# Performance work log

Measured on AMD Instinct MI355X. Metric: run time of the kernel, lower is better.

## Reference

```python
import jax, jax.numpy as jnp
import numpy as np

D_MODEL = 1024
NUM_HEADS = 16
D_K = D_MODEL // NUM_HEADS
D_FF = 4096
EPS = 1e-5


def _layer_norm(x, g, b):
    mu = jnp.mean(x, axis=-1, keepdims=True)
    var = jnp.mean(jnp.square(x - mu), axis=-1, keepdims=True)
    return (x - mu) * jax.lax.rsqrt(var + EPS) * g + b


def setup_inputs() -> dict:
    key = jax.random.key(0)
    ks = jax.random.split(key, 16)
    s = 0.02
    inp = {
        "x": jax.random.normal(ks[0], (2, 2048, D_MODEL), dtype=jnp.float32),
        # attention projections, torch Linear convention: W [out, in]
        "wq": jax.random.normal(ks[1], (D_MODEL, D_MODEL), dtype=jnp.float32) * s,
        "bq": jnp.zeros((D_MODEL,), jnp.float32),
        "wk": jax.random.normal(ks[2], (D_MODEL, D_MODEL), dtype=jnp.float32) * s,
        "bk": jnp.zeros((D_MODEL,), jnp.float32),
        "wv": jax.random.normal(ks[3], (D_MODEL, D_MODEL), dtype=jnp.float32) * s,
        "bv": jnp.zeros((D_MODEL,), jnp.float32),
        "wo": jax.random.normal(ks[4], (D_MODEL, D_MODEL), dtype=jnp.float32) * s,
        "bo": jnp.zeros((D_MODEL,), jnp.float32),
        "ln1_g": jnp.ones((D_MODEL,), jnp.float32),
        "ln1_b": jnp.zeros((D_MODEL,), jnp.float32),
        "w1": jax.random.normal(ks[5], (D_FF, D_MODEL), dtype=jnp.float32) * s,
        "b1": jnp.zeros((D_FF,), jnp.float32),
        "w2": jax.random.normal(ks[6], (D_MODEL, D_FF), dtype=jnp.float32) * s,
        "b2": jnp.zeros((D_MODEL,), jnp.float32),
        "ln2_g": jnp.ones((D_MODEL,), jnp.float32),
        "ln2_b": jnp.zeros((D_MODEL,), jnp.float32),
    }
    return inp


def reference(x, wq, bq, wk, bk, wv, bv, wo, bo, ln1_g, ln1_b,
              w1, b1, w2, b2, ln2_g, ln2_b):
    B, S, D = x.shape
    H, Dk = NUM_HEADS, D_K
    # projections -> [B, H, S, Dk]
    q = (x @ wq.T + bq).reshape(B, S, H, Dk).transpose(0, 2, 1, 3)
    k = (x @ wk.T + bk).reshape(B, S, H, Dk).transpose(0, 2, 1, 3)
    v = (x @ wv.T + bv).reshape(B, S, H, Dk).transpose(0, 2, 1, 3)
    # explicit [B,H,S,S] scores (faithful to source, memory-bound)
    scores = jnp.einsum("bhqd,bhkd->bhqk", q, k) / jnp.sqrt(jnp.float32(Dk))
    attn = jax.nn.softmax(scores, axis=-1)
    ctx = jnp.einsum("bhqk,bhkd->bhqd", attn, v)
    ctx = ctx.transpose(0, 2, 1, 3).reshape(B, S, D)
    attn_out = _layer_norm(ctx @ wo.T + bo + x, ln1_g, ln1_b)
    # feed-forward (post-LN residual), GELU (erf, torch default)
    h = jax.nn.gelu(attn_out @ w1.T + b1, approximate=False)
    ff = h @ w2.T + b2
    return _layer_norm(ff + attn_out, ln2_g, ln2_b)
```

## Files before the change

### kernel.cpp

```cpp
#include <hip/hip_runtime.h>
#include <math.h>

#define DM   1024
#define SL   2048
#define NB   2
#define NH   16
#define DKH  64
#define DFF  4096
#define NTOK 4096

typedef unsigned short u16;
typedef unsigned int u32;
typedef __attribute__((ext_vector_type(8))) short bf16x8;
typedef __attribute__((ext_vector_type(4))) float f32x4;
typedef __attribute__((ext_vector_type(16))) float f32x16;

typedef __attribute__((address_space(1))) void gvoid;
typedef __attribute__((address_space(3))) void lvoid;

#define QSCALE 0.18033688011112042f

__device__ __forceinline__ u16 f2bf(float f) {
  union { float f; unsigned u; } v; v.f = f;
  unsigned r = (v.u + 0x7fffu + ((v.u >> 16) & 1u)) >> 16;
  return (u16)r;
}
__device__ __forceinline__ float bf2f(u16 h) {
  union { unsigned u; float f; } v; v.u = ((unsigned)h) << 16; return v.f;
}
__device__ __forceinline__ void gld16(const u16* g, u16* l) {
  __builtin_amdgcn_global_load_lds((gvoid*)g, (lvoid*)l, 16, 0, 0);
}

__global__ __launch_bounds__(256)
void cvt_all(const float* __restrict__ x,  const float* __restrict__ wq,
             const float* __restrict__ wk, const float* __restrict__ wv,
             const float* __restrict__ wo, const float* __restrict__ w1,
             const float* __restrict__ w2,
             u16* __restrict__ xb, u16* __restrict__ wqb, u16* __restrict__ wkb,
             u16* __restrict__ wvb, u16* __restrict__ wob, u16* __restrict__ w1b,
             u16* __restrict__ w2b) {
  const int total = 4194304;
  for (int i = blockIdx.x * blockDim.x + threadIdx.x; i < total;
       i += gridDim.x * blockDim.x) {
    const float* src; u16* dst; int off;
    if      (i < 1048576) { src = x;  dst = xb;  off = i; }
    else if (i < 1310720) { src = wq; dst = wqb; off = i - 1048576; }
    else if (i < 1572864) { src = wk; dst = wkb; off = i - 1310720; }
    else if (i < 1835008) { src = wv; dst = wvb; off = i - 1572864; }
    else if (i < 2097152) { src = wo; dst = wob; off = i - 1835008; }
    else if (i < 3145728) { src = w1; dst = w1b; off = i - 2097152; }
    else                  { src = w2; dst = w2b; off = i - 3145728; }
    float4 v = ((const float4*)src)[off];
    ushort4 o = { f2bf(v.x), f2bf(v.y), f2bf(v.z), f2bf(v.w) };
    ((ushort4*)dst)[off] = o;
  }
}

#define BM 128
#define BN 128
#define BK 64

template <int EPI>
__global__ __launch_bounds__(256, 2)
void gemm_bt(const u16* __restrict__ A, const u16* __restrict__ W,
             const float* __restrict__ bias, const float* __restrict__ residf,
             const u16* __restrict__ residb, void* __restrict__ out,
             int M, int N, int K) {
  __shared__ u16 smem[2][2][BM * BK];
  const int tid = threadIdx.x;
  const int lane = tid & 63;
  const int wid  = tid >> 6;
  const int r16  = lane & 15;
  const int hi   = lane >> 4;
  const int wm = wid >> 1, wn = wid & 1;

  const int nwg = gridDim.x * gridDim.y;
  const int lid = blockIdx.y * 32 + blockIdx.x;
  const int l2  = (lid & 7) * (nwg >> 3) + (lid >> 3);
  const int bm  = (l2 & 31) * BM;
  const int bn  = (l2 >> 5) * BN;

  const int srow  = tid >> 3;
  const int sslot = (tid & 7) ^ (srow & 7);
  const size_t aoff = (size_t)(bm + srow) * K + sslot * 8;
  const size_t boff = (size_t)(bn + srow) * K + sslot * 8;

  f32x4 acc[4][4] = {};
  const int nk = K / BK;
  int cur = 0;

  auto STAGE = [&](int buf, int kt) {
    const u16* ga = A + aoff + kt * BK;
    const u16* gb = W + boff + kt * BK;
    u16* la = &smem[buf][0][wid * 512];
    u16* lb = &smem[buf][1][wid * 512];
#pragma unroll
    for (int i = 0; i < 4; ++i) {
      gld16(ga + (size_t)i * 32 * K, la + i * 2048);
      gld16(gb + (size_t)i * 32 * K, lb + i * 2048);
    }
  };

  STAGE(0, 0);
  __syncthreads();

  for (int kt = 0; kt < nk; ++kt) {
    if (kt + 1 < nk) STAGE(cur ^ 1, kt + 1);
    const u16* la = &smem[cur][0][0];
    const u16* lb = &smem[cur][1][0];
#pragma unroll
    for (int kk = 0; kk < 2; ++kk) {
      const int swz = ((kk * 4 + hi) ^ (r16 & 7)) * 8;
      bf16x8 af[4], bfr[4];
#pragma unroll
      for (int i = 0; i < 4; ++i)
        af[i] = *(const bf16x8*)&la[(wm * 64 + i * 16 + r16) * 64 + swz];
#pragma unroll
      for (int j = 0; j < 4; ++j)
        bfr[j] = *(const bf16x8*)&lb[(wn * 64 + j * 16 + r16) * 64 + swz];
      __builtin_amdgcn_s_setprio(1);
#pragma unroll
      for (int i = 0; i < 4; ++i)
#pragma unroll
        for (int j = 0; j < 4; ++j)
          acc[i][j] = __builtin_amdgcn_mfma_f32_16x16x32_bf16(af[i], bfr[j],
                                                              acc[i][j], 0, 0, 0);
      __builtin_amdgcn_s_setprio(0);
    }
    __syncthreads();
    cur ^= 1;
  }

#pragma unroll
  for (int i = 0; i < 4; ++i) {
#pragma unroll
    for (int j = 0; j < 4; ++j) {
      const int c  = bn + wn * 64 + j * 16 + r16;
      const int r0 = bm + wm * 64 + i * 16 + hi * 4;
      const float bv = bias[c];
#pragma unroll
      for (int rr = 0; rr < 4; ++rr) {
        const int r = r0 + rr;
        float v = acc[i][j][rr] + bv;
        if (EPI == 3) {
          ((u16*)out)[(size_t)r * N + c] = f2bf(v + residf[(size_t)r * N + c]);
        } else if (EPI == 4) {
          const float gl = 0.5f * v * (1.0f + erff(v * 0.7071067811865475f));
          ((u16*)out)[(size_t)r * N + c] = f2bf(gl);
        } else {
          ((u16*)out)[(size_t)r * N + c] =
              f2bf(v + bf2f(residb[(size_t)r * N + c]));
        }
      }
    }
  }
}

__global__ __launch_bounds__(256, 2)
void gemm_qkv(const u16* __restrict__ A, const u16* __restrict__ wq,
              const u16* __restrict__ wk, const u16* __restrict__ wv,
              const float* __restrict__ bq, const float* __restrict__ bk,
              const float* __restrict__ bv,
              u16* __restrict__ qo, u16* __restrict__ ko, u16* __restrict__ vo) {
  __shared__ u16 smem[2][2][BM * BK];
  const int tid = threadIdx.x;
  const int lane = tid & 63;
  const int wid  = tid >> 6;
  const int r16  = lane & 15;
  const int hi   = lane >> 4;
  const int wm = wid >> 1, wn = wid & 1;

  const int lid = blockIdx.y * 32 + blockIdx.x;
  const int l2  = (lid & 7) * 96 + (lid >> 3);
  const int bm  = (l2 & 31) * BM;
  const int by  = l2 >> 5;
  const int sel = by >> 3;
  const int bn  = (by & 7) * BN;
  const u16* W = sel == 0 ? wq : sel == 1 ? wk : wv;
  const float* bias = sel == 0 ? bq : sel == 1 ? bk : bv;
  const int K = DM, N = DM;

  const int srow  = tid >> 3;
  const int sslot = (tid & 7) ^ (srow & 7);
  const size_t aoff = (size_t)(bm + srow) * K + sslot * 8;
  const size_t boff = (size_t)(bn + srow) * K + sslot * 8;

  f32x4 acc[4][4] = {};
  int cur = 0;

  auto STAGE = [&](int buf, int kt) {
    const u16* ga = A + aoff + kt * BK;
    const u16* gb = W + boff + kt * BK;
    u16* la = &smem[buf][0][wid * 512];
    u16* lb = &smem[buf][1][wid * 512];
#pragma unroll
    for (int i = 0; i < 4; ++i) {
      gld16(ga + (size_t)i * 32 * K, la + i * 2048);
      gld16(gb + (size_t)i * 32 * K, lb + i * 2048);
    }
  };

  STAGE(0, 0);
  __syncthreads();

  for (int kt = 0; kt < 16; ++kt) {
    if (kt + 1 < 16) STAGE(cur ^ 1, kt + 1);
    const u16* la = &smem[cur][0][0];
    const u16* lb = &smem[cur][1][0];
#pragma unroll
    for (int kk = 0; kk < 2; ++kk) {
      const int swz = ((kk * 4 + hi) ^ (r16 & 7)) * 8;
      bf16x8 af[4], bfr[4];
#pragma unroll
      for (int i = 0; i < 4; ++i)
        af[i] = *(const bf16x8*)&la[(wm * 64 + i * 16 + r16) * 64 + swz];
#pragma unroll
      for (int j = 0; j < 4; ++j)
        bfr[j] = *(const bf16x8*)&lb[(wn * 64 + j * 16 + r16) * 64 + swz];
      __builtin_amdgcn_s_setprio(1);
#pragma unroll
      for (int i = 0; i < 4; ++i)
#pragma unroll
        for (int j = 0; j < 4; ++j)
          acc[i][j] = __builtin_amdgcn_mfma_f32_16x16x32_bf16(af[i], bfr[j],
                                                              acc[i][j], 0, 0, 0);
      __builtin_amdgcn_s_setprio(0);
    }
    __syncthreads();
    cur ^= 1;
  }

#pragma unroll
  for (int i = 0; i < 4; ++i) {
#pragma unroll
    for (int j = 0; j < 4; ++j) {
      const int c  = bn + wn * 64 + j * 16 + r16;
      const int r0 = bm + wm * 64 + i * 16 + hi * 4;
      const float bvv = bias[c];
#pragma unroll
      for (int rr = 0; rr < 4; ++rr) {
        const int r = r0 + rr;
        const float v = acc[i][j][rr] + bvv;
        if (sel == 0) {
          qo[(size_t)r * N + c] = f2bf(v * QSCALE);
        } else if (sel == 1) {
          ko[(size_t)r * N + c] = f2bf(v);
        } else {
          const int b = r >> 11, s = r & 2047;
          const int hh = c >> 6, dk = c & 63;
          vo[((size_t)((b * NH + hh) * DKH + dk)) * SL + s] = f2bf(v);
        }
      }
    }
  }
}

__global__ __launch_bounds__(256, 2)
void attn(const u16* __restrict__ q, const u16* __restrict__ k,
          const u16* __restrict__ vt, u16* __restrict__ ctx) {
  __shared__ u16 kl[2][64 * 64];
  __shared__ u16 vl[2][64 * 64];

  const int tid = threadIdx.x;
  const int lane = tid & 63, wid = tid >> 6;
  const int l31 = lane & 31, h = lane >> 5;
  const int rs = l31 & 7;

  const int lid = blockIdx.y * 32 + blockIdx.x;
  const int rr_ = lid & 31;
  const int bh = (rr_ & 7) * 4 + (rr_ >> 3);
  const int qb = lid >> 5;
  const int b = bh >> 4, hh = bh & 15;
  const int qg = qb * 128 + wid * 32 + l31;

  bf16x8 qf[4];
#pragma unroll
  for (int kq = 0; kq < 4; ++kq)
    qf[kq] = *(const bf16x8*)(q + (size_t)(b * SL + qg) * DM + hh * DKH +
                              kq * 16 + h * 8);

  f32x16 o0 = {}, o1 = {};
  float mrun = -1e30f, lrun = 0.f;

  const int srow  = tid >> 3;
  const int sslot = (tid & 7) ^ (srow & 7);

  auto STAGE = [&](int buf, int t) {
    const u16* gk = k + (size_t)(b * SL + t * 64 + srow) * DM + hh * DKH + sslot * 8;
    const u16* gv = vt + (size_t)(bh * DKH + srow) * SL + t * 64 + sslot * 8;
    u16* lk = &kl[buf][wid * 512];
    u16* lv = &vl[buf][wid * 512];
#pragma unroll
    for (int i = 0; i < 2; ++i) {
      gld16(gk + (size_t)i * 32 * DM, lk + i * 2048);
      gld16(gv + (size_t)i * 32 * SL, lv + i * 2048);
    }
  };

  auto TILE = [&](int buf) {
    const u16* lk = kl[buf];
    const u16* lv = vl[buf];
    f32x16 s0 = {}, s1 = {};
    __builtin_amdgcn_s_setprio(1);
#pragma unroll
    for (int kq = 0; kq < 4; ++kq) {
      const int ls = 2 * kq + h;
      bf16x8 k0 = *(const bf16x8*)&lk[l31 * 64 + ((ls ^ rs) * 8)];
      bf16x8 k1 = *(const bf16x8*)&lk[(l31 + 32) * 64 + ((ls ^ rs) * 8)];
      s0 = __builtin_amdgcn_mfma_f32_32x32x16_bf16(k0, qf[kq], s0, 0, 0, 0);
      s1 = __builtin_amdgcn_mfma_f32_32x32x16_bf16(k1, qf[kq], s1, 0, 0, 0);
    }
    __builtin_amdgcn_s_setprio(0);

    float mx = fmaxf(s0[0], s0[1]);
#pragma unroll
    for (int r = 2; r < 16; ++r) mx = fmaxf(mx, s0[r]);
#pragma unroll
    for (int r = 0; r < 16; ++r) mx = fmaxf(mx, s1[r]);
    {
      float ta = mx, tb = mx;
      asm volatile("v_permlane32_swap_b32 %0, %1" : "+v"(ta), "+v"(tb));
      mx = fmaxf(ta, tb);
    }
    if (!__all(mx <= mrun + 11.0f)) {
      const float mn = fmaxf(mrun, mx);
      const float al = __builtin_amdgcn_exp2f(mrun - mn);
      mrun = mn;
      lrun *= al;
      o0 *= al; o1 *= al;
    }
    float lsum = 0.f;
#pragma unroll
    for (int r = 0; r < 16; ++r) {
      s0[r] = __builtin_amdgcn_exp2f(s0[r] - mrun); lsum += s0[r];
    }
#pragma unroll
    for (int r = 0; r < 16; ++r) {
      s1[r] = __builtin_amdgcn_exp2f(s1[r] - mrun); lsum += s1[r];
    }
    lrun += lsum;

    u32 A[16];
#pragma unroll
    for (int r = 0; r < 8; ++r)
      asm("v_cvt_pk_bf16_f32 %0, %1, %2"
          : "=v"(A[r]) : "v"(s0[2 * r]), "v"(s0[2 * r + 1]));
#pragma unroll
    for (int r = 0; r < 8; ++r)
      asm("v_cvt_pk_bf16_f32 %0, %1, %2"
          : "=v"(A[8 + r]) : "v"(s1[2 * r]), "v"(s1[2 * r + 1]));
#pragma unroll
    for (int g = 0; g < 4; ++g) {
      asm volatile("v_permlane32_swap_b32 %0, %1" : "+v"(A[4 * g + 0]), "+v"(A[4 * g + 2]));
      asm volatile("v_permlane32_swap_b32 %0, %1" : "+v"(A[4 * g + 1]), "+v"(A[4 * g + 3]));
    }

    __builtin_amdgcn_s_setprio(1);
#pragma unroll
    for (int ks = 0; ks < 4; ++ks) {
      union { u32 u[4]; bf16x8 hv; } pb;
      pb.u[0] = A[4 * ks + 0]; pb.u[1] = A[4 * ks + 1];
      pb.u[2] = A[4 * ks + 2]; pb.u[3] = A[4 * ks + 3];
      const int ls = 2 * ks + h;
      bf16x8 v0 = *(const bf16x8*)&lv[l31 * 64 + ((ls ^ rs) * 8)];
      bf16x8 v1 = *(const bf16x8*)&lv[(l31 + 32) * 64 + ((ls ^ rs) * 8)];
      o0 = __builtin_amdgcn_mfma_f32_32x32x16_bf16(v0, pb.hv, o0, 0, 0, 0);
      o1 = __builtin_amdgcn_mfma_f32_32x32x16_bf16(v1, pb.hv, o1, 0, 0, 0);
    }
    __builtin_amdgcn_s_setprio(0);
  };

  STAGE(0, 0);
  __syncthreads();
  int cur = 0;
  for (int t = 0; t < SL / 64; ++t) {
    if (t + 1 < SL / 64) STAGE(cur ^ 1, t + 1);
    TILE(cur);
    __syncthreads();
    cur ^= 1;
  }

  float ta = lrun, tb = lrun;
  asm volatile("v_permlane32_swap_b32 %0, %1" : "+v"(ta), "+v"(tb));
  const float rl = 1.f / (ta + tb);
  const size_t obase = (size_t)(b * SL + qg) * DM + hh * DKH;
#pragma unroll
  for (int df = 0; df < 2; ++df) {
#pragma unroll
    for (int r2 = 0; r2 < 4; ++r2) {
      const int dk0 = 8 * r2 + 4 * h + 32 * df;
      ushort4 st;
      if (df == 0) {
        st.x = f2bf(o0[4 * r2 + 0] * rl); st.y = f2bf(o0[4 * r2 + 1] * rl);
        st.z = f2bf(o0[4 * r2 + 2] * rl); st.w = f2bf(o0[4 * r2 + 3] * rl);
      } else {
        st.x = f2bf(o1[4 * r2 + 0] * rl); st.y = f2bf(o1[4 * r2 + 1] * rl);
        st.z = f2bf(o1[4 * r2 + 2] * rl); st.w = f2bf(o1[4 * r2 + 3] * rl);
      }
      *(ushort4*)(ctx + obase + dk0) = st;
    }
  }
}

template <int INBF>
__global__ __launch_bounds__(256)
void ln_k(const void* __restrict__ inp, const float* __restrict__ g,
          const float* __restrict__ be, float* __restrict__ outf,
          u16* __restrict__ outb) {
  const int row = blockIdx.x;
  const int tid = threadIdx.x;
  float4 x4;
  if (INBF) {
    ushort4 h4 = ((const ushort4*)((const u16*)inp + (size_t)row * DM))[tid];
    x4.x = bf2f(h4.x); x4.y = bf2f(h4.y); x4.z = bf2f(h4.z); x4.w = bf2f(h4.w);
  } else {
    x4 = ((const float4*)((const float*)inp + (size_t)row * DM))[tid];
  }
  float s  = x4.x + x4.y + x4.z + x4.w;
  float s2 = x4.x * x4.x + x4.y * x4.y + x4.z * x4.z + x4.w * x4.w;
#pragma unroll
  for (int d = 1; d < 64; d <<= 1) {
    s  += __shfl_xor(s, d);
    s2 += __shfl_xor(s2, d);
  }
  __shared__ float ps[8];
  const int wid = tid >> 6, lane = tid & 63;
  if (lane == 0) { ps[wid] = s; ps[wid + 4] = s2; }
  __syncthreads();
  const float S  = ps[0] + ps[1] + ps[2] + ps[3];
  const float S2 = ps[4] + ps[5] + ps[6] + ps[7];
  const float mu = S * (1.f / DM);
  const float var = S2 * (1.f / DM) - mu * mu;
  const float rstd = 1.f / sqrtf(var + 1e-5f);
  const float4 gv = ((const float4*)g)[tid];
  const float4 bv = ((const float4*)be)[tid];
  float4 o;
  o.x = (x4.x - mu) * rstd * gv.x + bv.x;
  o.y = (x4.y - mu) * rstd * gv.y + bv.y;
  o.z = (x4.z - mu) * rstd * gv.z + bv.z;
  o.w = (x4.w - mu) * rstd * gv.w + bv.w;
  if (outf) ((float4*)(outf + (size_t)row * DM))[tid] = o;
  if (outb) {
    ushort4 ob = { f2bf(o.x), f2bf(o.y), f2bf(o.z), f2bf(o.w) };
    ((ushort4*)(outb + (size_t)row * DM))[tid] = ob;
  }
}

extern "C" void kernel_launch(void* const* d_in, const int* in_sizes, int n_in,
                              void* d_out, int out_size, void* d_ws, size_t ws_size,
                              hipStream_t stream) {
  const float* x   = (const float*)d_in[0];
  const float* wq  = (const float*)d_in[1];
  const float* bq  = (const float*)d_in[2];
  const float* wk  = (const float*)d_in[3];
  const float* bk  = (const float*)d_in[4];
  const float* wv  = (const float*)d_in[5];
  const float* bv  = (const float*)d_in[6];
  const float* wo  = (const float*)d_in[7];
  const float* bo  = (const float*)d_in[8];
  const float* g1  = (const float*)d_in[9];
  const float* be1 = (const float*)d_in[10];
  const float* w1  = (const float*)d_in[11];
  const float* b1  = (const float*)d_in[12];
  const float* w2  = (const float*)d_in[13];
  const float* b2  = (const float*)d_in[14];
  const float* g2  = (const float*)d_in[15];
  const float* be2 = (const float*)d_in[16];

  if (ws_size < ((size_t)80 << 20)) return;

  char* ws = (char*)d_ws;
  u16*  xb   = (u16*)(ws);
  u16*  wqb  = (u16*)(ws + ((size_t)8  << 20));
  u16*  wkb  = (u16*)(ws + ((size_t)10 << 20));
  u16*  wvb  = (u16*)(ws + ((size_t)12 << 20));
  u16*  wob  = (u16*)(ws + ((size_t)14 << 20));
  u16*  w1b  = (u16*)(ws + ((size_t)16 << 20));
  u16*  w2b  = (u16*)(ws + ((size_t)24 << 20));
  u16*  qbuf = (u16*)(ws + ((size_t)32 << 20));
  u16*  kbuf = (u16*)(ws + ((size_t)40 << 20));
  u16*  vtb  = (u16*)(ws + ((size_t)48 << 20));
  u16*  ctx  = (u16*)(ws + ((size_t)56 << 20));
  u16*  oresb = (u16*)(ws + ((size_t)64 << 20));
  u16*  ffb   = (u16*)(ws + ((size_t)72 << 20));
  u16*  aob  = xb;
  u16*  hb   = qbuf;

  float* out = (float*)d_out;
  dim3 blk(256);

  cvt_all<<<2048, blk, 0, stream>>>(x, wq, wk, wv, wo, w1, w2,
                                    xb, wqb, wkb, wvb, wob, w1b, w2b);
  gemm_qkv<<<dim3(32, 24), blk, 0, stream>>>(xb, wqb, wkb, wvb, bq, bk, bv,
                                             qbuf, kbuf, vtb);
  attn<<<dim3(32, 16), blk, 0, stream>>>(qbuf, kbuf, vtb, ctx);
  gemm_bt<3><<<dim3(32, 8), blk, 0, stream>>>(ctx, wob, bo, x, nullptr, oresb,
                                              NTOK, DM, DM);
  ln_k<1><<<4096, blk, 0, stream>>>(oresb, g1, be1, nullptr, aob);
  gemm_bt<4><<<dim3(32, 32), blk, 0, stream>>>(aob, w1b, b1, nullptr, nullptr,
                                               hb, NTOK, DFF, DM);
  gemm_bt<5><<<dim3(32, 8), blk, 0, stream>>>(hb, w2b, b2, nullptr, aob, ffb,
                                              NTOK, DM, DFF);
  ln_k<1><<<4096, blk, 0, stream>>>(ffb, g2, be2, out, nullptr);
}
```

Before: 250.4 us.

## Use 128x64 tiles for N=1024 GEMMs and drop block-index swizzling

The output-projection and FFN2 GEMMs now use 128x64 tiles with each wave covering 32 rows, doubling their grid to 512 workgroups, and raise launch bounds to 3 blocks per CU. This is meant to fix under-occupancy, since the old 256-block grid filled the GPU only once. All GEMM and attention kernels also replace the L2-grouping block remap with direct blockIdx mapping. That may reduce cache locality, and the smaller tiles lower data reuse per block.

Result: no change. 247.5 us (-1.2%).

```diff
diff --git a/kernel.cpp b/kernel.cpp
--- a/kernel.cpp
+++ b/kernel.cpp
@@ -58,48 +58,49 @@
 }
 
 #define BM 128
-#define BN 128
 #define BK 64
 
 template <int EPI>
-__global__ __launch_bounds__(256, 2)
+__global__ __launch_bounds__(256, (EPI == 4) ? 2 : 3)
 void gemm_bt(const u16* __restrict__ A, const u16* __restrict__ W,
              const float* __restrict__ bias, const float* __restrict__ residf,
              const u16* __restrict__ residb, void* __restrict__ out,
              int M, int N, int K) {
-  __shared__ u16 smem[2][2][BM * BK];
+  constexpr int BNT = (EPI == 4) ? 128 : 64;
+  constexpr int MFR = (BNT == 128) ? 4 : 2;
+  __shared__ u16 smemA[2][BM * BK];
+  __shared__ u16 smemB[2][BNT * BK];
+
   const int tid = threadIdx.x;
   const int lane = tid & 63;
   const int wid  = tid >> 6;
   const int r16  = lane & 15;
   const int hi   = lane >> 4;
-  const int wm = wid >> 1, wn = wid & 1;
-
-  const int nwg = gridDim.x * gridDim.y;
-  const int lid = blockIdx.y * 32 + blockIdx.x;
-  const int l2  = (lid & 7) * (nwg >> 3) + (lid >> 3);
-  const int bm  = (l2 & 31) * BM;
-  const int bn  = (l2 >> 5) * BN;
+  const int wm = (BNT == 128) ? (wid >> 1) : wid;
+  const int wn = (BNT == 128) ? (wid & 1) : 0;
+  const int bm = blockIdx.x * BM;
+  const int bn = blockIdx.y * BNT;
 
   const int srow  = tid >> 3;
   const int sslot = (tid & 7) ^ (srow & 7);
   const size_t aoff = (size_t)(bm + srow) * K + sslot * 8;
   const size_t boff = (size_t)(bn + srow) * K + sslot * 8;
 
-  f32x4 acc[4][4] = {};
+  f32x4 acc[MFR][4] = {};
   const int nk = K / BK;
   int cur = 0;
 
   auto STAGE = [&](int buf, int kt) {
     const u16* ga = A + aoff + kt * BK;
     const u16* gb = W + boff + kt * BK;
-    u16* la = &smem[buf][0][wid * 512];
-    u16* lb = &smem[buf][1][wid * 512];
-#pragma unroll
-    for (int i = 0; i < 4; ++i) {
+    u16* la = &smemA[buf][wid * 512];
+    u16* lb = &smemB[buf][wid * 512];
+#pragma unroll
+    for (int i = 0; i < 4; ++i)
       gld16(ga + (size_t)i * 32 * K, la + i * 2048);
+#pragma unroll
+    for (int i = 0; i < BNT / 32; ++i)
       gld16(gb + (size_t)i * 32 * K, lb + i * 2048);
-    }
   };
 
   STAGE(0, 0);
@@ -107,21 +108,21 @@
 
   for (int kt = 0; kt < nk; ++kt) {
     if (kt + 1 < nk) STAGE(cur ^ 1, kt + 1);
-    const u16* la = &smem[cur][0][0];
-    const u16* lb = &smem[cur][1][0];
+    const u16* la = &smemA[cur][0];
+    const u16* lb = &smemB[cur][0];
 #pragma unroll
     for (int kk = 0; kk < 2; ++kk) {
       const int swz = ((kk * 4 + hi) ^ (r16 & 7)) * 8;
-      bf16x8 af[4], bfr[4];
-#pragma unroll
-      for (int i = 0; i < 4; ++i)
-        af[i] = *(const bf16x8*)&la[(wm * 64 + i * 16 + r16) * 64 + swz];
+      bf16x8 af[MFR], bfr[4];
+#pragma unroll
+      for (int i = 0; i < MFR; ++i)
+        af[i] = *(const bf16x8*)&la[(wm * (MFR * 16) + i * 16 + r16) * 64 + swz];
 #pragma unroll
       for (int j = 0; j < 4; ++j)
         bfr[j] = *(const bf16x8*)&lb[(wn * 64 + j * 16 + r16) * 64 + swz];
       __builtin_amdgcn_s_setprio(1);
 #pragma unroll
-      for (int i = 0; i < 4; ++i)
+      for (int i = 0; i < MFR; ++i)
 #pragma unroll
         for (int j = 0; j < 4; ++j)
           acc[i][j] = __builtin_amdgcn_mfma_f32_16x16x32_bf16(af[i], bfr[j],
@@ -133,11 +134,11 @@
   }
 
 #pragma unroll
-  for (int i = 0; i < 4; ++i) {
+  for (int i = 0; i < MFR; ++i) {
 #pragma unroll
     for (int j = 0; j < 4; ++j) {
       const int c  = bn + wn * 64 + j * 16 + r16;
-      const int r0 = bm + wm * 64 + i * 16 + hi * 4;
+      const int r0 = bm + wm * (MFR * 16) + i * 16 + hi * 4;
       const float bv = bias[c];
 #pragma unroll
       for (int rr = 0; rr < 4; ++rr) {
@@ -170,13 +171,9 @@
   const int r16  = lane & 15;
   const int hi   = lane >> 4;
   const int wm = wid >> 1, wn = wid & 1;
-
-  const int lid = blockIdx.y * 32 + blockIdx.x;
-  const int l2  = (lid & 7) * 96 + (lid >> 3);
-  const int bm  = (l2 & 31) * BM;
-  const int by  = l2 >> 5;
-  const int sel = by >> 3;
-  const int bn  = (by & 7) * BN;
+  const int bm = blockIdx.x * BM;
+  const int sel = blockIdx.y >> 3;
+  const int bn  = (blockIdx.y & 7) * 128;
   const u16* W = sel == 0 ? wq : sel == 1 ? wk : wv;
   const float* bias = sel == 0 ? bq : sel == 1 ? bk : bv;
   const int K = DM, N = DM;
@@ -266,13 +263,8 @@
   const int lane = tid & 63, wid = tid >> 6;
   const int l31 = lane & 31, h = lane >> 5;
   const int rs = l31 & 7;
-
-  const int lid = blockIdx.y * 32 + blockIdx.x;
-  const int rr_ = lid & 31;
-  const int bh = (rr_ & 7) * 4 + (rr_ >> 3);
-  const int qb = lid >> 5;
-  const int b = bh >> 4, hh = bh & 15;
-  const int qg = qb * 128 + wid * 32 + l31;
+  const int bh = blockIdx.x, b = bh >> 4, hh = bh & 15;
+  const int qg = blockIdx.y * 128 + wid * 32 + l31;
 
   bf16x8 qf[4];
 #pragma unroll
@@ -495,12 +487,12 @@
   gemm_qkv<<<dim3(32, 24), blk, 0, stream>>>(xb, wqb, wkb, wvb, bq, bk, bv,
                                              qbuf, kbuf, vtb);
   attn<<<dim3(32, 16), blk, 0, stream>>>(qbuf, kbuf, vtb, ctx);
-  gemm_bt<3><<<dim3(32, 8), blk, 0, stream>>>(ctx, wob, bo, x, nullptr, oresb,
-                                              NTOK, DM, DM);
+  gemm_bt<3><<<dim3(32, 16), blk, 0, stream>>>(ctx, wob, bo, x, nullptr, oresb,
+                                               NTOK, DM, DM);
   ln_k<1><<<4096, blk, 0, stream>>>(oresb, g1, be1, nullptr, aob);
   gemm_bt<4><<<dim3(32, 32), blk, 0, stream>>>(aob, w1b, b1, nullptr, nullptr,
                                                hb, NTOK, DFF, DM);
-  gemm_bt<5><<<dim3(32, 8), blk, 0, stream>>>(hb, w2b, b2, nullptr, aob, ffb,
-                                              NTOK, DM, DFF);
+  gemm_bt<5><<<dim3(32, 16), blk, 0, stream>>>(hb, w2b, b2, nullptr, aob, ffb,
+                                               NTOK, DM, DFF);
   ln_k<1><<<4096, blk, 0, stream>>>(ffb, g2, be2, out, nullptr);
 }
```
